# Kernel optimization log

Hardware: AMD Instinct MI355X
Metric: run time of the kernel (lower is better)

Reference implementation:

```python
import jax, jax.numpy as jnp
import numpy as np

ND, NPR, DD, DP, LAT, AT, B = 2048, 2048, 128, 128, 128, 32, 16384


def setup_inputs():
    key = jax.random.key(0)
    ks = jax.random.split(key, 20)
    s = 0.05
    d = {}
    d["e_p_adj"] = (jax.random.uniform(ks[0], (ND, NPR)) < 0.05).astype(jnp.float32)
    d["e_e_adj"] = (jax.random.uniform(ks[1], (ND, ND)) < 0.05).astype(jnp.float32)
    d["p_p_adj"] = (jax.random.uniform(ks[2], (NPR, NPR)) < 0.05).astype(jnp.float32)
    d["input_disease"] = jax.random.randint(ks[3], (B,), 0, ND)
    d["input_drug"] = jax.random.randint(ks[4], (B,), 0, NPR)
    d["labels"] = jax.random.randint(ks[5], (B,), 0, 2)
    # learned parameters
    d["disease_emb"] = jax.random.normal(ks[6], (ND, DD)) * s
    d["drug_emb"] = jax.random.normal(ks[7], (NPR, DP)) * s
    d["Wdg"] = jax.random.normal(ks[8], (DP, LAT)) * s   # disease_gcn_w
    d["bdg_lin"] = jnp.zeros((LAT,))                      # Linear bias
    d["bdg"] = jnp.zeros((LAT,))                          # extra disease_gcn_b
    d["Wpg"] = jax.random.normal(ks[9], (DD, LAT)) * s   # drug_gcn_w
    d["bpg_lin"] = jnp.zeros((LAT,))
    d["bpg"] = jnp.zeros((LAT,))
    d["Wa1_d"] = jax.random.normal(ks[10], (DP + DD, AT)) * s  # concat [key(drug), query(disease)]
    d["ba1_d"] = jnp.zeros((AT,))
    d["Wa2_d"] = jax.random.normal(ks[11], (AT, 1)) * s
    d["ba2_d"] = jnp.zeros((1,))
    d["Wa1_p"] = jax.random.normal(ks[12], (DD + DP, AT)) * s  # concat [key(disease), query(drug)]
    d["ba1_p"] = jnp.zeros((AT,))
    d["Wa2_p"] = jax.random.normal(ks[13], (AT, 1)) * s
    d["ba2_p"] = jnp.zeros((1,))
    d["Wd2"] = jax.random.normal(ks[14], (DD, LAT)) * s  # disease_w2
    d["bd2"] = jnp.zeros((LAT,))
    d["Wp3"] = jax.random.normal(ks[15], (DP, LAT)) * s  # drug_w3
    d["bp3"] = jnp.zeros((LAT,))
    d["mlp_W1"] = jax.random.normal(ks[16], (LAT, DD)) * s
    d["mlp_b1"] = jnp.zeros((DD,))
    d["mlp_W2"] = jax.random.normal(ks[17], (DD, DD)) * s
    d["mlp_b2"] = jnp.zeros((DD,))
    d["Wpred"] = jax.random.normal(ks[18], (DD, 1)) * s
    d["bpred"] = jnp.zeros((1,))
    return d


def _attention_gcn(adj, other, selfe, W1, b1, W2, b2):
    # torch: concat([key=other, query=self]) -> Linear(W1) ; split W1 instead of
    # materializing the [Ns, No, Dk+Dq] concat tensor (same math, less HBM traffic)
    do = other.shape[1]
    ko = other @ W1[:do]              # [No, A]
    qs = selfe @ W1[do:]              # [Ns, A]
    h = jax.nn.relu(qs[:, None, :] + ko[None, :, :] + b1)   # [Ns, No, A]
    alpha = jax.nn.relu(jnp.squeeze(h @ W2, -1) + b2[0])    # [Ns, No]
    alpha = alpha * adj
    return jax.nn.softmax(alpha, axis=1) @ other            # [Ns, Do]


def _forward(e_p_adj, e_e_adj, p_p_adj, input_disease, input_drug, labels,
             disease_emb, drug_emb, Wdg, bdg_lin, bdg, Wpg, bpg_lin, bpg,
             Wa1_d, ba1_d, Wa2_d, ba2_d, Wa1_p, ba1_p, Wa2_p, ba2_p,
             Wd2, bd2, Wp3, bp3, mlp_W1, mlp_b1, mlp_W2, mlp_b2, Wpred, bpred):
    h_e_gcn = _attention_gcn(e_p_adj, drug_emb, disease_emb, Wa1_d, ba1_d, Wa2_d, ba2_d)
    h_e_gcn = h_e_gcn @ Wdg + bdg_lin + bdg
    h_p_gcn = _attention_gcn(e_p_adj.T, disease_emb, drug_emb, Wa1_p, ba1_p, Wa2_p, ba2_p)
    h_p_gcn = h_p_gcn @ Wpg + bpg_lin + bpg
    # disease knn branch
    deg_d = jnp.sum(e_e_adj, axis=1, keepdims=True) + 1e-8
    h_e_e = ((e_e_adj @ disease_emb) / deg_d) @ Wd2 + bd2
    h_e = jax.nn.selu(h_e_gcn + h_e_e)
    # drug knn branch
    deg_p = jnp.sum(p_p_adj, axis=1, keepdims=True) + 1e-8
    h_p_p = ((p_p_adj @ drug_emb) / deg_p) @ Wp3 + bp3
    h_p = jax.nn.selu(h_p_gcn + h_p_p)
    # pair prediction MLP
    x = h_e[input_disease] * h_p[input_drug]                # [B, LAT]
    x = jax.nn.selu(x @ mlp_W1 + mlp_b1)
    x = jax.nn.selu(x @ mlp_W2 + mlp_b2)
    z = jnp.squeeze(x @ Wpred, -1) + bpred[0]               # [B]
    y = labels.astype(jnp.float32)
    # BCEWithLogitsLoss (stable), mean reduction
    loss = jnp.mean(jnp.maximum(z, 0.0) - z * y + jnp.log1p(jnp.exp(-jnp.abs(z))))
    return (loss, jax.nn.sigmoid(z))


def reference(e_p_adj, e_e_adj, p_p_adj, input_disease, input_drug, labels,
              disease_emb, drug_emb, Wdg, bdg_lin, bdg, Wpg, bpg_lin, bpg,
              Wa1_d, ba1_d, Wa2_d, ba2_d, Wa1_p, ba1_p, Wa2_p, ba2_p,
              Wd2, bd2, Wp3, bp3, mlp_W1, mlp_b1, mlp_W2, mlp_b2, Wpred, bpred):
    return _forward(e_p_adj, e_e_adj, p_p_adj, input_disease, input_drug, labels,
                    disease_emb, drug_emb, Wdg, bdg_lin, bdg, Wpg, bpg_lin, bpg,
                    Wa1_d, ba1_d, Wa2_d, ba2_d, Wa1_p, ba1_p, Wa2_p, ba2_p,
                    Wd2, bd2, Wp3, bp3, mlp_W1, mlp_b1, mlp_W2, mlp_b2, Wpred, bpred)
```

## Files before the change

kernel.cpp:

```cpp
#include <hip/hip_runtime.h>

#define ND   2048
#define BB   16384

typedef unsigned short u16;
typedef unsigned int u32;
typedef __attribute__((ext_vector_type(8))) short short8;
typedef __attribute__((ext_vector_type(4))) float f32x4;

__device__ inline float bf2f(u16 u) {
    union { u32 i; float f; } v; v.i = ((u32)u) << 16; return v.f;
}
__device__ inline u16 f2bf(float f) {
    union { float f; u32 i; } v; v.f = f;
    u32 i = v.i + 0x7fffu + ((v.i >> 16) & 1u);
    return (u16)(i >> 16);
}
__device__ inline float seluf(float x) {
    const float sc = 1.0507009873554805f, al = 1.6732632423543772f;
    return x > 0.f ? sc * x : sc * al * expm1f(x);
}
__device__ inline short8 packbf8(float4 f0, float4 f1) {
    short8 a;
    a[0] = (short)f2bf(f0.x); a[1] = (short)f2bf(f0.y);
    a[2] = (short)f2bf(f0.z); a[3] = (short)f2bf(f0.w);
    a[4] = (short)f2bf(f1.x); a[5] = (short)f2bf(f1.y);
    a[6] = (short)f2bf(f1.z); a[7] = (short)f2bf(f1.w);
    return a;
}

__global__ void detectk(const void* __restrict__ demb, u32* __restrict__ flag) {
    const u16* p = (const u16*)demb;
    int tid = threadIdx.x;
    int sane = 0;
    #pragma unroll
    for (int i = 0; i < 2; i++) {
        u16 u = p[4 * tid + 2 * i];
        int e = (u >> 7) & 0xFF;
        if (u == 0 || (e >= 0x66 && e <= 0x8C)) sane++;
    }
    __shared__ int red[256];
    red[tid] = sane; __syncthreads();
    for (int o = 128; o > 0; o >>= 1) {
        if (tid < o) red[tid] += red[tid + o];
        __syncthreads();
    }
    if (tid == 0) flag[0] = (red[0] < 300) ? 1u : 0u;
}

#define NSEG 26
struct CvtArgs { const void* src[NSEG]; int off[NSEG]; int n[NSEG]; };

__global__ __launch_bounds__(256) void cvtk(CvtArgs a, u16* __restrict__ base,
                                            const u32* __restrict__ flag) {
    int seg = blockIdx.y;
    int n = a.n[seg];
    const void* s = a.src[seg];
    u16* d = base + a.off[seg];
    bool f32 = flag[0] != 0;
    int stride = gridDim.x * blockDim.x;
    for (int i = blockIdx.x * blockDim.x + threadIdx.x; i < n; i += stride)
        d[i] = f32 ? f2bf(((const float*)s)[i]) : ((const u16*)s)[i];
}

__device__ inline void tpose_body(const u16* in, int R, int C,
                                  u16* out, int ldo, int ooff,
                                  u16 (*tile)[33]) {
    int c0 = blockIdx.x * 32, r0 = blockIdx.y * 32;
    int x = c0 + threadIdx.x;
    for (int i = threadIdx.y; i < 32; i += 8) {
        int r = r0 + i;
        tile[i][threadIdx.x] = (r < R && x < C) ? in[(size_t)r * C + x] : (u16)0;
    }
    __syncthreads();
    int rr = r0 + threadIdx.x;
    for (int i = threadIdx.y; i < 32; i += 8) {
        int cc = c0 + i;
        if (cc < C && rr < R) out[(size_t)cc * ldo + ooff + rr] = tile[threadIdx.x][i];
    }
}

__global__ void tpose_embs(const u16* __restrict__ demb, const u16* __restrict__ pemb,
                           u16* __restrict__ disT, u16* __restrict__ drugT) {
    __shared__ u16 tile[32][33];
    if (blockIdx.z == 0) tpose_body(demb, ND, 128, disT, ND, 0, tile);
    else                 tpose_body(pemb, ND, 128, drugT, ND, 0, tile);
}

__global__ void tpose_smalls(const u16* s0, const u16* s1, const u16* s2,
                             const u16* s3, const u16* s4, const u16* s5,
                             u16* W1T, u16* W2T, u16* WcTe, u16* WcTp) {
    __shared__ u16 tile[32][33];
    const u16* in; u16* out; int ldo, ooff;
    switch (blockIdx.z) {
        case 0:  in = s0; out = W1T;  ldo = 128; ooff = 0;   break;
        case 1:  in = s1; out = W2T;  ldo = 128; ooff = 0;   break;
        case 2:  in = s2; out = WcTe; ldo = 256; ooff = 0;   break;
        case 3:  in = s3; out = WcTe; ldo = 256; ooff = 128; break;
        case 4:  in = s4; out = WcTp; ldo = 256; ooff = 0;   break;
        default: in = s5; out = WcTp; ldo = 256; ooff = 128; break;
    }
    tpose_body(in, 128, 128, out, ldo, ooff, tile);
}

__global__ void biasc(const u16* a0, const u16* a1, const u16* a2, u16* o0,
                      const u16* b0, const u16* b1, const u16* b2, u16* o1) {
    int t = threadIdx.x;
    o0[t] = f2bf(bf2f(a0[t]) + bf2f(a1[t]) + bf2f(a2[t]));
    o1[t] = f2bf(bf2f(b0[t]) + bf2f(b1[t]) + bf2f(b2[t]));
}

__global__ __launch_bounds__(256) void degk(
    const void* __restrict__ e_e, float* __restrict__ dinv_e,
    const void* __restrict__ p_p, float* __restrict__ dinv_p,
    const u32* __restrict__ flag) {
    int row = blockIdx.x, tid = threadIdx.x;
    const void* ab = blockIdx.y ? p_p : e_e;
    float* o = blockIdx.y ? dinv_p : dinv_e;
    bool f32 = flag[0] != 0;
    float s = 0.f;
    if (f32) {
        const float4* a4 = (const float4*)((const float*)ab + (size_t)row * 2048) + tid * 2;
        float4 v0 = a4[0], v1 = a4[1];
        s = v0.x + v0.y + v0.z + v0.w + v1.x + v1.y + v1.z + v1.w;
    } else {
        const uint4* a4 = (const uint4*)((const u16*)ab + (size_t)row * 2048) + tid;
        uint4 v = a4[0];
        u32 u[4] = {v.x, v.y, v.z, v.w};
        #pragma unroll
        for (int c = 0; c < 4; c++)
            s += bf2f((u16)(u[c] & 0xffff)) + bf2f((u16)(u[c] >> 16));
    }
    __shared__ float red[256];
    red[tid] = s; __syncthreads();
    for (int ofs = 128; ofs > 0; ofs >>= 1) {
        if (tid < ofs) red[tid] += red[tid + ofs];
        __syncthreads();
    }
    if (tid == 0) o[row] = 1.f / (red[0] + 1e-8f);
}

__global__ __launch_bounds__(128) void koqs(
    const u16* __restrict__ demb, const u16* __restrict__ pemb,
    const u16* __restrict__ Wa1d, const u16* __restrict__ ba1d,
    const u16* __restrict__ Wa1p, const u16* __restrict__ ba1p,
    float* __restrict__ ko_d, float* __restrict__ qs_d,
    float* __restrict__ ko_p, float* __restrict__ qs_p) {
    int row = blockIdx.x, m = blockIdx.y, tid = threadIdx.x;
    const u16* src; const u16* W; const u16* bias; float* out;
    switch (m) {
        case 0:  src = pemb; W = Wa1d;            bias = nullptr; out = ko_d; break;
        case 1:  src = demb; W = Wa1d + 128 * 32; bias = ba1d;    out = qs_d; break;
        case 2:  src = demb; W = Wa1p;            bias = nullptr; out = ko_p; break;
        default: src = pemb; W = Wa1p + 128 * 32; bias = ba1p;    out = qs_p; break;
    }
    __shared__ float x[128];
    __shared__ float red[128];
    x[tid] = bf2f(src[(size_t)row * 128 + tid]);
    __syncthreads();
    int a = tid & 31, part = tid >> 5;
    float s = 0.f;
    #pragma unroll
    for (int k = 0; k < 32; k++) s += x[part * 32 + k] * bf2f(W[(part * 32 + k) * 32 + a]);
    red[tid] = s;
    __syncthreads();
    if (part == 0) {
        float t = red[a] + red[a + 32] + red[a + 64] + red[a + 96];
        if (bias) t += bf2f(bias[a]);
        out[(size_t)row * 32 + a] = t;
    }
}

struct AW {
    const float* qs[2]; const float* ko[2];
    const u16* w2[2]; const u16* b2[2];
    u16* outw[2]; float* sums[2];
    int transposed[2];
};

__global__ __launch_bounds__(256, 4) void attnw6(AW a, const void* __restrict__ adj,
                                                 const u32* __restrict__ flag) {
    __shared__ float tile[32][257];
    __shared__ float wpart[4][32];
    int z = blockIdx.z;
    int tid = threadIdx.x;
    int lane = tid & 63, wv = tid >> 6;
    int jl = wv * 64 + lane;
    int jbase = blockIdx.x * 256;
    int j = jbase + jl;
    int p0 = blockIdx.y * 32;
    bool f32a = flag[0] != 0;
    bool tr = a.transposed[z] != 0;
    const float* adjf = (const float*)adj;
    const u16*   adjh = (const u16*)adj;

    float kv[32];
    {
        const float4* kp = (const float4*)(a.ko[z] + (size_t)j * 32);
        #pragma unroll
        for (int qd = 0; qd < 8; qd++) {
            float4 v = kp[qd];
            kv[qd * 4 + 0] = v.x; kv[qd * 4 + 1] = v.y;
            kv[qd * 4 + 2] = v.z; kv[qd * 4 + 3] = v.w;
        }
    }
    float w2v[32];
    #pragma unroll
    for (int i2 = 0; i2 < 32; i2++) w2v[i2] = bf2f(a.w2[z][i2]);
    float b2 = bf2f(a.b2[z][0]);
    const float* qs = a.qs[z];
    u16* outw = a.outw[z];

    if (tr) {
        if (f32a) {
            const float4* src = (const float4*)(adjf + (size_t)(jbase + tid) * 2048 + p0);
            #pragma unroll
            for (int q8 = 0; q8 < 8; q8++) {
                float4 v = src[q8];
                tile[q8 * 4 + 0][tid] = v.x; tile[q8 * 4 + 1][tid] = v.y;
                tile[q8 * 4 + 2][tid] = v.z; tile[q8 * 4 + 3][tid] = v.w;
            }
        } else {
            const uint4* src = (const uint4*)(adjh + (size_t)(jbase + tid) * 2048 + p0);
            #pragma unroll
            for (int q8 = 0; q8 < 4; q8++) {
                uint4 v = src[q8];
                u32 uu[4] = {v.x, v.y, v.z, v.w};
                #pragma unroll
                for (int c = 0; c < 4; c++) {
                    tile[q8 * 8 + c * 2 + 0][tid] = bf2f((u16)(uu[c] & 0xffff));
                    tile[q8 * 8 + c * 2 + 1][tid] = bf2f((u16)(uu[c] >> 16));
                }
            }
        }
        __syncthreads();
    }

    #pragma unroll 1
    for (int pl = 0; pl < 32; pl++) {
        int row = p0 + pl;
        const float* qrow = qs + (size_t)row * 32;
        float s = 0.f;
        #pragma unroll
        for (int aa = 0; aa < 32; aa++)
            s += fmaxf(qrow[aa] + kv[aa], 0.f) * w2v[aa];
        s = fmaxf(s + b2, 0.f);
        float av = tr ? tile[pl][jl]
                      : (f32a ? adjf[(size_t)row * 2048 + j]
                              : bf2f(adjh[(size_t)row * 2048 + j]));
        float e = __expf(s * av);
        outw[(size_t)row * 2048 + j] = f2bf(e);
        float t = e;
        #pragma unroll
        for (int o = 32; o > 0; o >>= 1) t += __shfl_down(t, o, 64);
        if (lane == 0) wpart[wv][pl] = t;
    }
    __syncthreads();
    if (tid < 32)
        a.sums[z][(size_t)blockIdx.x * 2048 + p0 + tid] =
            wpart[0][tid] + wpart[1][tid] + wpart[2][tid] + wpart[3][tid];
}

struct GD4 {
    const void* A[4]; const u16* BT[4]; u16* C[4];
    const u16* bias[4]; const float* rs[4];
    int lda[4], ldb[4], ldc[4], coff[4], kiters[4], act[4], araw[4], rsmode[4];
};

#define PADK 136

__global__ __launch_bounds__(256, 2) void gemmL(GD4 g, const u32* __restrict__ flag) {
    __shared__ __align__(16) u16 As[16][PADK];
    __shared__ __align__(16) u16 Bs[128][PADK];
    int z = blockIdx.y;
    bool af32 = g.araw[z] && (flag[0] != 0);
    const void* A = g.A[z];
    const u16* BT = g.BT[z];
    int lda = g.lda[z], ldb = g.ldb[z];
    int kiters = g.kiters[z];
    int tid = threadIdx.x;
    int lane = tid & 63, wv = tid >> 6;
    int mrow = lane & 15, quad = lane >> 4;
    int m0 = blockIdx.x * 16;
    int c0 = wv * 32;
    int sr = tid >> 4, sk = (tid & 15) * 8;
    f32x4 acc0 = {0.f, 0.f, 0.f, 0.f}, acc1 = {0.f, 0.f, 0.f, 0.f};

    short8 ra, rb[8];
    auto ldstage = [&](int kb) {
        if (af32) {
            const float* A32 = (const float*)A;
            const float4* p = (const float4*)(A32 + (size_t)(m0 + sr) * lda + kb + sk);
            float4 f0 = p[0], f1 = p[1];
            ra = packbf8(f0, f1);
        } else {
            ra = *(const short8*)((const u16*)A + (size_t)(m0 + sr) * lda + kb + sk);
        }
        const u16* bbase = BT + (size_t)sr * ldb + kb + sk;
        #pragma unroll
        for (int i = 0; i < 8; i++)
            rb[i] = *(const short8*)(bbase + (size_t)i * 16 * ldb);
    };
    auto ststage = [&]() {
        *(short8*)(&As[sr][sk]) = ra;
        #pragma unroll
        for (int i = 0; i < 8; i++)
            *(short8*)(&Bs[i * 16 + sr][sk]) = rb[i];
    };
    auto compute = [&]() {
        #pragma unroll
        for (int ks = 0; ks < 4; ks++) {
            short8 af = *(const short8*)(&As[mrow][ks * 32 + quad * 8]);
            short8 b0 = *(const short8*)(&Bs[c0 + mrow][ks * 32 + quad * 8]);
            short8 b1 = *(const short8*)(&Bs[c0 + 16 + mrow][ks * 32 + quad * 8]);
            acc0 = __builtin_amdgcn_mfma_f32_16x16x32_bf16(af, b0, acc0, 0, 0, 0);
            acc1 = __builtin_amdgcn_mfma_f32_16x16x32_bf16(af, b1, acc1, 0, 0, 0);
        }
    };

    ldstage(0);
    #pragma unroll 1
    for (int it = 0; it < kiters - 1; ++it) {
        ststage();
        __syncthreads();
        ldstage((it + 1) * 128);
        compute();
        __syncthreads();
    }
    ststage();
    __syncthreads();
    compute();

    const float* rs = g.rs[z];
    int rsmode = g.rsmode[z];
    const u16* bi = g.bias[z];
    u16* C = g.C[z];
    int ldc = g.ldc[z], coff = g.coff[z], act = g.act[z];
    int n0 = c0 + mrow, n1 = n0 + 16;
    float bv0 = bi ? bf2f(bi[n0]) : 0.f;
    float bv1 = bi ? bf2f(bi[n1]) : 0.f;
    #pragma unroll
    for (int r = 0; r < 4; r++) {
        int row = m0 + quad * 4 + r;
        float v0 = acc0[r], v1 = acc1[r];
        if (rsmode == 1) { float sc = rs[row]; v0 *= sc; v1 *= sc; }
        else if (rsmode == 2) {
            float t = 0.f;
            #pragma unroll
            for (int p = 0; p < 8; p++) t += rs[row + p * 2048];
            float sc = 1.f / t;
            v0 *= sc; v1 *= sc;
        }
        v0 += bv0; v1 += bv1;
        if (act) { v0 = seluf(v0); v1 = seluf(v1); }
        C[(size_t)row * ldc + coff + n0] = f2bf(v0);
        C[(size_t)row * ldc + coff + n1] = f2bf(v1);
    }
}

__global__ __launch_bounds__(256) void xbuild(
    const u16* __restrict__ he, const u16* __restrict__ hp,
    const int* __restrict__ di, const int* __restrict__ dr, u16* __restrict__ X) {
    int idx = blockIdx.x * 256 + threadIdx.x;
    int d2 = idx & 63;
    int b = idx >> 6;
    int ia = di[b], ic = dr[b];
    u32 ue = ((const u32*)he)[ia * 64 + d2];
    u32 up = ((const u32*)hp)[ic * 64 + d2];
    float lo = bf2f((u16)(ue & 0xffff)) * bf2f((u16)(up & 0xffff));
    float hi = bf2f((u16)(ue >> 16)) * bf2f((u16)(up >> 16));
    ((u32*)X)[idx] = (u32)f2bf(lo) | ((u32)f2bf(hi) << 16);
}

__global__ __launch_bounds__(256) void zloss(
    const u16* __restrict__ X2, const u16* __restrict__ wpred,
    const u16* __restrict__ bpred, const int* __restrict__ labels,
    float* __restrict__ out, float* __restrict__ part) {
    __shared__ float wp[128];
    __shared__ float ls[256];
    int tid = threadIdx.x;
    if (tid < 128) wp[tid] = bf2f(wpred[tid]);
    __syncthreads();
    int b = blockIdx.x * 256 + tid;
    const uint4* xp = (const uint4*)(X2 + (size_t)b * 128);
    float z = 0.f;
    #pragma unroll
    for (int i = 0; i < 16; i++) {
        uint4 q = xp[i];
        u32 u[4] = {q.x, q.y, q.z, q.w};
        #pragma unroll
        for (int c = 0; c < 4; c++) {
            z += bf2f((u16)(u[c] & 0xffff)) * wp[i * 8 + c * 2];
            z += bf2f((u16)(u[c] >> 16)) * wp[i * 8 + c * 2 + 1];
        }
    }
    z += bf2f(bpred[0]);
    out[1 + b] = 1.f / (1.f + __expf(-z));
    float y = (float)labels[b];
    ls[tid] = fmaxf(z, 0.f) - z * y + log1pf(__expf(-fabsf(z)));
    __syncthreads();
    for (int o = 128; o > 0; o >>= 1) {
        if (tid < o) ls[tid] += ls[tid + o];
        __syncthreads();
    }
    if (tid == 0) part[blockIdx.x] = ls[0];
}

__global__ void finloss(const float* __restrict__ part, float* __restrict__ out) {
    __shared__ float s[64];
    s[threadIdx.x] = part[threadIdx.x];
    __syncthreads();
    for (int o = 32; o > 0; o >>= 1) {
        if (threadIdx.x < o) s[threadIdx.x] += s[threadIdx.x + o];
        __syncthreads();
    }
    if (threadIdx.x == 0) out[0] = s[0] * (1.f / 16384.f);
}

extern "C" void kernel_launch(void* const* d_in, const int* in_sizes, int n_in,
                              void* d_out, int out_size, void* d_ws, size_t ws_size,
                              hipStream_t stream) {
    const void* e_p_adj = d_in[0];
    const void* e_e_adj = d_in[1];
    const void* p_p_adj = d_in[2];
    const int* in_dis  = (const int*)d_in[3];
    const int* in_drug = (const int*)d_in[4];
    const int* labels  = (const int*)d_in[5];
    float* out = (float*)d_out;

    char* ws = (char*)d_ws;
    size_t off = 0;
    auto take = [&](size_t bytes) { char* p = ws + off; off = (off + bytes + 255) & ~(size_t)255; return p; };
    u16*   Wbuf  = (u16*)take((size_t)2048 * 2048 * 2);
    u16*   drugT = (u16*)take((size_t)128 * 2048 * 2);
    u16*   disT  = (u16*)take((size_t)128 * 2048 * 2);
    float* ko_d  = (float*)take((size_t)2048 * 32 * 4);
    float* qs_d  = (float*)take((size_t)2048 * 32 * 4);
    float* ko_p  = (float*)take((size_t)2048 * 32 * 4);
    float* qs_p  = (float*)take((size_t)2048 * 32 * 4);
    u16*   A_e   = (u16*)take((size_t)2048 * 256 * 2);
    u16*   A_p   = (u16*)take((size_t)2048 * 256 * 2);
    u16*   WcTe  = (u16*)take((size_t)128 * 256 * 2);
    u16*   WcTp  = (u16*)take((size_t)128 * 256 * 2);
    u16*   W1T   = (u16*)take((size_t)128 * 128 * 2);
    u16*   W2T   = (u16*)take((size_t)128 * 128 * 2);
    u16*   b_e   = (u16*)take(256);
    u16*   b_p   = (u16*)take(256);
    u16*   h_e   = (u16*)take((size_t)2048 * 128 * 2);
    u16*   h_p   = (u16*)take((size_t)2048 * 128 * 2);
    float* dinv_e = (float*)take(2048 * 4);
    float* dinv_p = (float*)take(2048 * 4);
    float* sumsD  = (float*)take(8 * 2048 * 4);
    float* sumsP  = (float*)take(8 * 2048 * 4);
    float* part  = (float*)take(64 * 4);
    u16*   canon = (u16*)take((size_t)700000 * 2);
    u32*   flag  = (u32*)take(256);
    bool dual = (ws_size > off) && (ws_size - off) >= ((size_t)2048 * 2048 * 2 + 512);
    u16*   Wbuf2 = dual ? (u16*)take((size_t)2048 * 2048 * 2) : Wbuf;
    u16* X  = Wbuf;
    u16* X1 = Wbuf + (size_t)BB * 128;
    u16* X2 = drugT;

    const int segidx[NSEG] = {6, 7, 14, 18, 8, 22, 11, 24, 26, 28,
                              15, 16, 17, 19, 20, 21,
                              9, 10, 12, 13, 23, 25, 27, 29, 30, 31};
    const int segn[NSEG]   = {262144, 262144, 8192, 8192, 16384, 16384, 16384, 16384, 16384, 16384,
                              32, 32, 1, 32, 32, 1,
                              128, 128, 128, 128, 128, 128, 128, 128, 128, 1};
    CvtArgs ca;
    u16* cp[NSEG];
    {
        int o = 0;
        for (int i = 0; i < NSEG; i++) {
            ca.src[i] = d_in[segidx[i]];
            ca.off[i] = o;
            ca.n[i] = segn[i];
            cp[i] = canon + o;
            o += (segn[i] + 15) & ~15;
        }
    }
    u16 *cdemb = cp[0], *cpemb = cp[1], *cWa1d = cp[2], *cWa1p = cp[3];
    u16 *cWdg = cp[4], *cWd2 = cp[5], *cWpg = cp[6], *cWp3 = cp[7];
    u16 *cW1 = cp[8], *cW2 = cp[9];
    u16 *cba1d = cp[10], *cWa2d = cp[11], *cba2d = cp[12];
    u16 *cba1p = cp[13], *cWa2p = cp[14], *cba2p = cp[15];
    u16 *cbdg_lin = cp[16], *cbdg = cp[17], *cbpg_lin = cp[18], *cbpg = cp[19];
    u16 *cbd2 = cp[20], *cbp3 = cp[21], *cmb1 = cp[22], *cmb2 = cp[23];
    u16 *cWpred = cp[24], *cbpred = cp[25];

    detectk<<<1, 256, 0, stream>>>(d_in[6], flag);
    cvtk<<<dim3(64, NSEG), 256, 0, stream>>>(ca, canon, flag);

    tpose_embs<<<dim3(4, 64, 2), dim3(32, 8), 0, stream>>>(cdemb, cpemb, disT, drugT);
    tpose_smalls<<<dim3(4, 4, 6), dim3(32, 8), 0, stream>>>(
        cW1, cW2, cWdg, cWd2, cWpg, cWp3, W1T, W2T, WcTe, WcTp);
    biasc<<<1, 128, 0, stream>>>(cbdg_lin, cbdg, cbd2, b_e, cbpg_lin, cbpg, cbp3, b_p);
    degk<<<dim3(2048, 2), 256, 0, stream>>>(e_e_adj, dinv_e, p_p_adj, dinv_p, flag);
    koqs<<<dim3(2048, 4), 128, 0, stream>>>(cdemb, cpemb, cWa1d, cba1d, cWa1p, cba1p,
                                            ko_d, qs_d, ko_p, qs_p);

    auto setd = [](GD4& g, int z, const void* A, int lda, const u16* BT, int ldb,
                   u16* C, int ldc, int coff, int ki, const u16* bi,
                   const float* rs, int act, int araw, int rm) {
        g.A[z] = A; g.lda[z] = lda; g.BT[z] = BT; g.ldb[z] = ldb;
        g.C[z] = C; g.ldc[z] = ldc; g.coff[z] = coff; g.kiters[z] = ki;
        g.bias[z] = bi; g.rs[z] = rs; g.act[z] = act; g.araw[z] = araw; g.rsmode[z] = rm;
    };
    auto mkaw = [](const float* qs0, const float* ko0, const u16* w20, const u16* b20,
                   u16* o0, float* s0, int t0,
                   const float* qs1, const float* ko1, const u16* w21, const u16* b21,
                   u16* o1, float* s1, int t1) {
        AW a;
        a.qs[0] = qs0; a.ko[0] = ko0; a.w2[0] = w20; a.b2[0] = b20;
        a.outw[0] = o0; a.sums[0] = s0; a.transposed[0] = t0;
        a.qs[1] = qs1; a.ko[1] = ko1; a.w2[1] = w21; a.b2[1] = b21;
        a.outw[1] = o1; a.sums[1] = s1; a.transposed[1] = t1;
        return a;
    };

    if (dual) {
        AW aw = mkaw(qs_d, ko_d, cWa2d, cba2d, Wbuf, sumsD, 0,
                     qs_p, ko_p, cWa2p, cba2p, Wbuf2, sumsP, 1);
        attnw6<<<dim3(8, 64, 2), 256, 0, stream>>>(aw, e_p_adj, flag);
        GD4 g;
        setd(g, 0, Wbuf, 2048, drugT, 2048, A_e, 256, 0, 16, nullptr, sumsD, 0, 0, 2);
        setd(g, 1, e_e_adj, 2048, disT, 2048, A_e, 256, 128, 16, nullptr, dinv_e, 0, 1, 1);
        setd(g, 2, Wbuf2, 2048, disT, 2048, A_p, 256, 0, 16, nullptr, sumsP, 0, 0, 2);
        setd(g, 3, p_p_adj, 2048, drugT, 2048, A_p, 256, 128, 16, nullptr, dinv_p, 0, 1, 1);
        gemmL<<<dim3(128, 4), 256, 0, stream>>>(g, flag);
    } else {
        AW aw1 = mkaw(qs_d, ko_d, cWa2d, cba2d, Wbuf, sumsD, 0,
                      qs_d, ko_d, cWa2d, cba2d, Wbuf, sumsD, 0);
        attnw6<<<dim3(8, 64, 1), 256, 0, stream>>>(aw1, e_p_adj, flag);
        GD4 g1;
        setd(g1, 0, Wbuf, 2048, drugT, 2048, A_e, 256, 0, 16, nullptr, sumsD, 0, 0, 2);
        setd(g1, 1, e_e_adj, 2048, disT, 2048, A_e, 256, 128, 16, nullptr, dinv_e, 0, 1, 1);
        setd(g1, 2, Wbuf, 2048, drugT, 2048, A_e, 256, 0, 16, nullptr, sumsD, 0, 0, 2);
        setd(g1, 3, Wbuf, 2048, drugT, 2048, A_e, 256, 0, 16, nullptr, sumsD, 0, 0, 2);
        gemmL<<<dim3(128, 2), 256, 0, stream>>>(g1, flag);
        AW aw2 = mkaw(qs_p, ko_p, cWa2p, cba2p, Wbuf, sumsP, 1,
                      qs_p, ko_p, cWa2p, cba2p, Wbuf, sumsP, 1);
        attnw6<<<dim3(8, 64, 1), 256, 0, stream>>>(aw2, e_p_adj, flag);
        GD4 g2;
        setd(g2, 0, Wbuf, 2048, disT, 2048, A_p, 256, 0, 16, nullptr, sumsP, 0, 0, 2);
        setd(g2, 1, p_p_adj, 2048, drugT, 2048, A_p, 256, 128, 16, nullptr, dinv_p, 0, 1, 1);
        setd(g2, 2, Wbuf, 2048, disT, 2048, A_p, 256, 0, 16, nullptr, sumsP, 0, 0, 2);
        setd(g2, 3, Wbuf, 2048, disT, 2048, A_p, 256, 0, 16, nullptr, sumsP, 0, 0, 2);
        gemmL<<<dim3(128, 2), 256, 0, stream>>>(g2, flag);
    }

    {
        GD4 g;
        setd(g, 0, A_e, 256, WcTe, 256, h_e, 128, 0, 2, b_e, nullptr, 1, 0, 0);
        setd(g, 1, A_p, 256, WcTp, 256, h_p, 128, 0, 2, b_p, nullptr, 1, 0, 0);
        setd(g, 2, A_e, 256, WcTe, 256, h_e, 128, 0, 2, b_e, nullptr, 1, 0, 0);
        setd(g, 3, A_e, 256, WcTe, 256, h_e, 128, 0, 2, b_e, nullptr, 1, 0, 0);
        gemmL<<<dim3(128, 2), 256, 0, stream>>>(g, flag);
    }

    xbuild<<<4096, 256, 0, stream>>>(h_e, h_p, in_dis, in_drug, X);
    {
        GD4 g;
        setd(g, 0, X, 128, W1T, 128, X1, 128, 0, 1, cmb1, nullptr, 1, 0, 0);
        setd(g, 1, X, 128, W1T, 128, X1, 128, 0, 1, cmb1, nullptr, 1, 0, 0);
        setd(g, 2, X, 128, W1T, 128, X1, 128, 0, 1, cmb1, nullptr, 1, 0, 0);
        setd(g, 3, X, 128, W1T, 128, X1, 128, 0, 1, cmb1, nullptr, 1, 0, 0);
        gemmL<<<dim3(1024, 1), 256, 0, stream>>>(g, flag);
    }
    {
        GD4 g;
        setd(g, 0, X1, 128, W2T, 128, X2, 128, 0, 1, cmb2, nullptr, 1, 0, 0);
        setd(g, 1, X1, 128, W2T, 128, X2, 128, 0, 1, cmb2, nullptr, 1, 0, 0);
        setd(g, 2, X1, 128, W2T, 128, X2, 128, 0, 1, cmb2, nullptr, 1, 0, 0);
        setd(g, 3, X1, 128, W2T, 128, X2, 128, 0, 1, cmb2, nullptr, 1, 0, 0);
        gemmL<<<dim3(1024, 1), 256, 0, stream>>>(g, flag);
    }

    zloss<<<64, 256, 0, stream>>>(X2, cWpred, cbpred, labels, out, part);
    finloss<<<1, 64, 0, stream>>>(part, out);
}
```

Baseline: 256.6 us.

## Replace dense attention and adjacency GEMMs with CSR sparse aggregation

```diff
diff --git a/kernel.cpp b/kernel.cpp
--- a/kernel.cpp
+++ b/kernel.cpp
@@ -78,13 +78,6 @@
         int cc = c0 + i;
         if (cc < C && rr < R) out[(size_t)cc * ldo + ooff + rr] = tile[threadIdx.x][i];
     }
-}
-
-__global__ void tpose_embs(const u16* __restrict__ demb, const u16* __restrict__ pemb,
-                           u16* __restrict__ disT, u16* __restrict__ drugT) {
-    __shared__ u16 tile[32][33];
-    if (blockIdx.z == 0) tpose_body(demb, ND, 128, disT, ND, 0, tile);
-    else                 tpose_body(pemb, ND, 128, drugT, ND, 0, tile);
 }
 
 __global__ void tpose_smalls(const u16* s0, const u16* s1, const u16* s2,
@@ -103,41 +96,45 @@
     tpose_body(in, 128, 128, out, ldo, ooff, tile);
 }
 
+__global__ __launch_bounds__(256) void colsump(const u16* __restrict__ demb,
+                                               const u16* __restrict__ pemb,
+                                               float* __restrict__ part) {
+    int m = blockIdx.y;
+    const u16* e = m ? pemb : demb;
+    int t = threadIdx.x;
+    int c2 = t & 63, rg = t >> 6;
+    int r0 = blockIdx.x * 64;
+    float s0 = 0.f, s1 = 0.f;
+    for (int i = 0; i < 16; i++) {
+        u32 v = *(const u32*)(e + (size_t)(r0 + i * 4 + rg) * 128 + c2 * 2);
+        s0 += bf2f((u16)(v & 0xffffu));
+        s1 += bf2f((u16)(v >> 16));
+    }
+    __shared__ float t0[256], t1[256];
+    t0[t] = s0; t1[t] = s1;
+    __syncthreads();
+    if (t < 64) {
+        float a0 = t0[t] + t0[t + 64] + t0[t + 128] + t0[t + 192];
+        float a1 = t1[t] + t1[t + 64] + t1[t + 128] + t1[t + 192];
+        part[(size_t)m * 4096 + blockIdx.x * 128 + t * 2 + 0] = a0;
+        part[(size_t)m * 4096 + blockIdx.x * 128 + t * 2 + 1] = a1;
+    }
+}
+
 __global__ void biasc(const u16* a0, const u16* a1, const u16* a2, u16* o0,
-                      const u16* b0, const u16* b1, const u16* b2, u16* o1) {
+                      const u16* b0, const u16* b1, const u16* b2, u16* o1,
+                      const float* __restrict__ part,
+                      float* __restrict__ csd, float* __restrict__ csp) {
     int t = threadIdx.x;
     o0[t] = f2bf(bf2f(a0[t]) + bf2f(a1[t]) + bf2f(a2[t]));
     o1[t] = f2bf(bf2f(b0[t]) + bf2f(b1[t]) + bf2f(b2[t]));
-}
-
-__global__ __launch_bounds__(256) void degk(
-    const void* __restrict__ e_e, float* __restrict__ dinv_e,
-    const void* __restrict__ p_p, float* __restrict__ dinv_p,
-    const u32* __restrict__ flag) {
-    int row = blockIdx.x, tid = threadIdx.x;
-    const void* ab = blockIdx.y ? p_p : e_e;
-    float* o = blockIdx.y ? dinv_p : dinv_e;
-    bool f32 = flag[0] != 0;
-    float s = 0.f;
-    if (f32) {
-        const float4* a4 = (const float4*)((const float*)ab + (size_t)row * 2048) + tid * 2;
-        float4 v0 = a4[0], v1 = a4[1];
-        s = v0.x + v0.y + v0.z + v0.w + v1.x + v1.y + v1.z + v1.w;
-    } else {
-        const uint4* a4 = (const uint4*)((const u16*)ab + (size_t)row * 2048) + tid;
-        uint4 v = a4[0];
-        u32 u[4] = {v.x, v.y, v.z, v.w};
-        #pragma unroll
-        for (int c = 0; c < 4; c++)
-            s += bf2f((u16)(u[c] & 0xffff)) + bf2f((u16)(u[c] >> 16));
-    }
-    __shared__ float red[256];
-    red[tid] = s; __syncthreads();
-    for (int ofs = 128; ofs > 0; ofs >>= 1) {
-        if (tid < ofs) red[tid] += red[tid + ofs];
-        __syncthreads();
-    }
-    if (tid == 0) o[row] = 1.f / (red[0] + 1e-8f);
+    float sd = 0.f, sp = 0.f;
+    for (int b = 0; b < 32; b++) {
+        sd += part[b * 128 + t];
+        sp += part[4096 + b * 128 + t];
+    }
+    csd[t] = sd;
+    csp[t] = sp;
 }
 
 __global__ __launch_bounds__(128) void koqs(
@@ -171,94 +168,133 @@
     }
 }
 
-struct AW {
-    const float* qs[2]; const float* ko[2];
-    const u16* w2[2]; const u16* b2[2];
-    u16* outw[2]; float* sums[2];
-    int transposed[2];
+struct CS {
+    const void* adj[3];
+    u16* ridx[3]; u32* rcnt[3];
+    u16* cidx; u32* ccnt;
 };
 
-__global__ __launch_bounds__(256, 4) void attnw6(AW a, const void* __restrict__ adj,
-                                                 const u32* __restrict__ flag) {
-    __shared__ float tile[32][257];
-    __shared__ float wpart[4][32];
-    int z = blockIdx.z;
+__global__ __launch_bounds__(256) void csrbuild(CS c, const u32* __restrict__ flag) {
+    int m = blockIdx.y, r = blockIdx.x, t = threadIdx.x;
+    bool f32 = flag[0] != 0;
+    __shared__ u32 lcnt;
+    if (t == 0) lcnt = 0;
+    __syncthreads();
+    float v[8];
+    int c0 = t * 8;
+    if (f32) {
+        const float4* p = (const float4*)((const float*)c.adj[m] + (size_t)r * 2048 + c0);
+        float4 x = p[0], y = p[1];
+        v[0] = x.x; v[1] = x.y; v[2] = x.z; v[3] = x.w;
+        v[4] = y.x; v[5] = y.y; v[6] = y.z; v[7] = y.w;
+    } else {
+        const uint4* p = (const uint4*)((const u16*)c.adj[m] + (size_t)r * 2048 + c0);
+        uint4 x = p[0];
+        u32 u[4] = {x.x, x.y, x.z, x.w};
+        #pragma unroll
+        for (int i = 0; i < 4; i++) {
+            v[2 * i + 0] = (u[i] & 0xffffu) ? 1.f : 0.f;
+            v[2 * i + 1] = (u[i] >> 16)     ? 1.f : 0.f;
+        }
+    }
+    u16* ridx = c.ridx[m] + (size_t)r * 2048;
+    #pragma unroll
+    for (int i = 0; i < 8; i++) {
+        if (v[i] != 0.f) {
+            u32 p = atomicAdd(&lcnt, 1u);
+            ridx[p] = (u16)(c0 + i);
+            if (m == 0) {
+                u32 q = atomicAdd(&c.ccnt[c0 + i], 1u);
+                c.cidx[(size_t)(c0 + i) * 2048 + q] = (u16)r;
+            }
+        }
+    }
+    __syncthreads();
+    if (t == 0) c.rcnt[m][r] = lcnt;
+}
+
+struct SP {
+    const u16* idx[4]; const u32* cnt[4];
+    const float* ko[4]; const float* qs[4];
+    const u16* w2[4]; const u16* b2[4];
+    const u16* emb[4]; const float* csum[4];
+    u16* out[4]; int ooff[4]; int attn[4];
+};
+
+__global__ __launch_bounds__(256) void spagg(SP a) {
+    int task = blockIdx.y;
     int tid = threadIdx.x;
-    int lane = tid & 63, wv = tid >> 6;
-    int jl = wv * 64 + lane;
-    int jbase = blockIdx.x * 256;
-    int j = jbase + jl;
-    int p0 = blockIdx.y * 32;
-    bool f32a = flag[0] != 0;
-    bool tr = a.transposed[z] != 0;
-    const float* adjf = (const float*)adj;
-    const u16*   adjh = (const u16*)adj;
-
-    float kv[32];
-    {
-        const float4* kp = (const float4*)(a.ko[z] + (size_t)j * 32);
+    int wv = tid >> 6, lane = tid & 63;
+    int r = blockIdx.x * 4 + wv;
+    const u16* idx = a.idx[task] + (size_t)r * 2048;
+    int nnz = (int)a.cnt[task][r];
+    int isat = a.attn[task];
+    const u16* emb = a.emb[task];
+    const float* ko = a.ko[task];
+
+    float qsr[32], w2h[32];
+    float b2v = 0.f;
+    if (isat) {
+        const float4* qp = (const float4*)(a.qs[task] + (size_t)r * 32);
         #pragma unroll
-        for (int qd = 0; qd < 8; qd++) {
-            float4 v = kp[qd];
-            kv[qd * 4 + 0] = v.x; kv[qd * 4 + 1] = v.y;
-            kv[qd * 4 + 2] = v.z; kv[qd * 4 + 3] = v.w;
-        }
-    }
-    float w2v[32];
-    #pragma unroll
-    for (int i2 = 0; i2 < 32; i2++) w2v[i2] = bf2f(a.w2[z][i2]);
-    float b2 = bf2f(a.b2[z][0]);
-    const float* qs = a.qs[z];
-    u16* outw = a.outw[z];
-
-    if (tr) {
-        if (f32a) {
-            const float4* src = (const float4*)(adjf + (size_t)(jbase + tid) * 2048 + p0);
-            #pragma unroll
-            for (int q8 = 0; q8 < 8; q8++) {
-                float4 v = src[q8];
-                tile[q8 * 4 + 0][tid] = v.x; tile[q8 * 4 + 1][tid] = v.y;
-                tile[q8 * 4 + 2][tid] = v.z; tile[q8 * 4 + 3][tid] = v.w;
+        for (int i = 0; i < 8; i++) {
+            float4 v = qp[i];
+            qsr[4 * i + 0] = v.x; qsr[4 * i + 1] = v.y;
+            qsr[4 * i + 2] = v.z; qsr[4 * i + 3] = v.w;
+        }
+        #pragma unroll
+        for (int i = 0; i < 32; i++) w2h[i] = bf2f(a.w2[task][i]);
+        b2v = bf2f(a.b2[task][0]);
+    }
+
+    float acc0 = 0.f, acc1 = 0.f, wsum = 0.f;
+
+    for (int base = 0; base < nnz; base += 64) {
+        int i = base + lane;
+        float w = 0.f;
+        int j = 0;
+        if (i < nnz) {
+            j = (int)idx[i];
+            if (isat) {
+                const float4* kp = (const float4*)(ko + (size_t)j * 32);
+                float s = 0.f;
+                #pragma unroll
+                for (int q = 0; q < 8; q++) {
+                    float4 kv = kp[q];
+                    s += fmaxf(qsr[4 * q + 0] + kv.x, 0.f) * w2h[4 * q + 0];
+                    s += fmaxf(qsr[4 * q + 1] + kv.y, 0.f) * w2h[4 * q + 1];
+                    s += fmaxf(qsr[4 * q + 2] + kv.z, 0.f) * w2h[4 * q + 2];
+                    s += fmaxf(qsr[4 * q + 3] + kv.w, 0.f) * w2h[4 * q + 3];
+                }
+                w = __expf(fmaxf(s + b2v, 0.f)) - 1.f;
+            } else {
+                w = 1.f;
             }
-        } else {
-            const uint4* src = (const uint4*)(adjh + (size_t)(jbase + tid) * 2048 + p0);
-            #pragma unroll
-            for (int q8 = 0; q8 < 4; q8++) {
-                uint4 v = src[q8];
-                u32 uu[4] = {v.x, v.y, v.z, v.w};
-                #pragma unroll
-                for (int c = 0; c < 4; c++) {
-                    tile[q8 * 8 + c * 2 + 0][tid] = bf2f((u16)(uu[c] & 0xffff));
-                    tile[q8 * 8 + c * 2 + 1][tid] = bf2f((u16)(uu[c] >> 16));
-                }
-            }
-        }
-        __syncthreads();
-    }
-
-    #pragma unroll 1
-    for (int pl = 0; pl < 32; pl++) {
-        int row = p0 + pl;
-        const float* qrow = qs + (size_t)row * 32;
-        float s = 0.f;
-        #pragma unroll
-        for (int aa = 0; aa < 32; aa++)
-            s += fmaxf(qrow[aa] + kv[aa], 0.f) * w2v[aa];
-        s = fmaxf(s + b2, 0.f);
-        float av = tr ? tile[pl][jl]
-                      : (f32a ? adjf[(size_t)row * 2048 + j]
-                              : bf2f(adjh[(size_t)row * 2048 + j]));
-        float e = __expf(s * av);
-        outw[(size_t)row * 2048 + j] = f2bf(e);
-        float t = e;
-        #pragma unroll
-        for (int o = 32; o > 0; o >>= 1) t += __shfl_down(t, o, 64);
-        if (lane == 0) wpart[wv][pl] = t;
-    }
-    __syncthreads();
-    if (tid < 32)
-        a.sums[z][(size_t)blockIdx.x * 2048 + p0 + tid] =
-            wpart[0][tid] + wpart[1][tid] + wpart[2][tid] + wpart[3][tid];
+        }
+        int cend = min(64, nnz - base);
+        #pragma unroll 4
+        for (int k = 0; k < cend; k++) {
+            float wk = __shfl(w, k);
+            int jk = __shfl(j, k);
+            u32 pe = *(const u32*)(emb + (size_t)jk * 128 + lane * 2);
+            acc0 = fmaf(wk, bf2f((u16)(pe & 0xffffu)), acc0);
+            acc1 = fmaf(wk, bf2f((u16)(pe >> 16)), acc1);
+            wsum += wk;
+        }
+    }
+
+    float v0, v1;
+    if (isat) {
+        float sc = 1.f / (2048.f + wsum);
+        v0 = (a.csum[task][lane * 2 + 0] + acc0) * sc;
+        v1 = (a.csum[task][lane * 2 + 1] + acc1) * sc;
+    } else {
+        float sc = 1.f / (wsum + 1e-8f);
+        v0 = acc0 * sc;
+        v1 = acc1 * sc;
+    }
+    u32 pk = (u32)f2bf(v0) | ((u32)f2bf(v1) << 16);
+    *(u32*)(a.out[task] + (size_t)r * 256 + a.ooff[task] + lane * 2) = pk;
 }
 
 struct GD4 {
@@ -431,13 +467,6 @@
     char* ws = (char*)d_ws;
     size_t off = 0;
     auto take = [&](size_t bytes) { char* p = ws + off; off = (off + bytes + 255) & ~(size_t)255; return p; };
-    u16*   Wbuf  = (u16*)take((size_t)2048 * 2048 * 2);
-    u16*   drugT = (u16*)take((size_t)128 * 2048 * 2);
-    u16*   disT  = (u16*)take((size_t)128 * 2048 * 2);
-    float* ko_d  = (float*)take((size_t)2048 * 32 * 4);
-    float* qs_d  = (float*)take((size_t)2048 * 32 * 4);
-    float* ko_p  = (float*)take((size_t)2048 * 32 * 4);
-    float* qs_p  = (float*)take((size_t)2048 * 32 * 4);
     u16*   A_e   = (u16*)take((size_t)2048 * 256 * 2);
     u16*   A_p   = (u16*)take((size_t)2048 * 256 * 2);
     u16*   WcTe  = (u16*)take((size_t)128 * 256 * 2);
@@ -448,18 +477,27 @@
     u16*   b_p   = (u16*)take(256);
     u16*   h_e   = (u16*)take((size_t)2048 * 128 * 2);
     u16*   h_p   = (u16*)take((size_t)2048 * 128 * 2);
-    float* dinv_e = (float*)take(2048 * 4);
-    float* dinv_p = (float*)take(2048 * 4);
-    float* sumsD  = (float*)take(8 * 2048 * 4);
-    float* sumsP  = (float*)take(8 * 2048 * 4);
+    float* ko_d  = (float*)take((size_t)2048 * 32 * 4);
+    float* qs_d  = (float*)take((size_t)2048 * 32 * 4);
+    float* ko_p  = (float*)take((size_t)2048 * 32 * 4);
+    float* qs_p  = (float*)take((size_t)2048 * 32 * 4);
+    float* cspart = (float*)take((size_t)2 * 32 * 128 * 4);
+    float* csd   = (float*)take(128 * 4);
+    float* csp   = (float*)take(128 * 4);
     float* part  = (float*)take(64 * 4);
+    u32*   flag  = (u32*)take(256);
     u16*   canon = (u16*)take((size_t)700000 * 2);
-    u32*   flag  = (u32*)take(256);
-    bool dual = (ws_size > off) && (ws_size - off) >= ((size_t)2048 * 2048 * 2 + 512);
-    u16*   Wbuf2 = dual ? (u16*)take((size_t)2048 * 2048 * 2) : Wbuf;
-    u16* X  = Wbuf;
-    u16* X1 = Wbuf + (size_t)BB * 128;
-    u16* X2 = drugT;
+    u16*   X     = (u16*)take((size_t)BB * 128 * 2);
+    u16*   X1    = (u16*)take((size_t)BB * 128 * 2);
+    u16*   X2    = (u16*)take((size_t)BB * 128 * 2);
+    u16*   idx0  = (u16*)take((size_t)2048 * 2048 * 2);
+    u16*   idx1  = (u16*)take((size_t)2048 * 2048 * 2);
+    u16*   idx2  = (u16*)take((size_t)2048 * 2048 * 2);
+    u16*   idx3  = (u16*)take((size_t)2048 * 2048 * 2);
+    u32*   cnt0  = (u32*)take(2048 * 4);
+    u32*   cnt2  = (u32*)take(2048 * 4);
+    u32*   cnt3  = (u32*)take(2048 * 4);
+    u32*   cntT  = (u32*)take(2048 * 4);
 
     const int segidx[NSEG] = {6, 7, 14, 18, 8, 22, 11, 24, 26, 28,
                               15, 16, 17, 19, 20, 21,
@@ -491,13 +529,40 @@
     detectk<<<1, 256, 0, stream>>>(d_in[6], flag);
     cvtk<<<dim3(64, NSEG), 256, 0, stream>>>(ca, canon, flag);
 
-    tpose_embs<<<dim3(4, 64, 2), dim3(32, 8), 0, stream>>>(cdemb, cpemb, disT, drugT);
+    hipMemsetAsync(cntT, 0, 2048 * sizeof(u32), stream);
+    {
+        CS cs;
+        cs.adj[0] = e_p_adj; cs.ridx[0] = idx0; cs.rcnt[0] = cnt0;
+        cs.adj[1] = e_e_adj; cs.ridx[1] = idx2; cs.rcnt[1] = cnt2;
+        cs.adj[2] = p_p_adj; cs.ridx[2] = idx3; cs.rcnt[2] = cnt3;
+        cs.cidx = idx1; cs.ccnt = cntT;
+        csrbuild<<<dim3(2048, 3), 256, 0, stream>>>(cs, flag);
+    }
+
+    colsump<<<dim3(32, 2), 256, 0, stream>>>(cdemb, cpemb, cspart);
     tpose_smalls<<<dim3(4, 4, 6), dim3(32, 8), 0, stream>>>(
         cW1, cW2, cWdg, cWd2, cWpg, cWp3, W1T, W2T, WcTe, WcTp);
-    biasc<<<1, 128, 0, stream>>>(cbdg_lin, cbdg, cbd2, b_e, cbpg_lin, cbpg, cbp3, b_p);
-    degk<<<dim3(2048, 2), 256, 0, stream>>>(e_e_adj, dinv_e, p_p_adj, dinv_p, flag);
+    biasc<<<1, 128, 0, stream>>>(cbdg_lin, cbdg, cbd2, b_e, cbpg_lin, cbpg, cbp3, b_p,
+                                 cspart, csd, csp);
     koqs<<<dim3(2048, 4), 128, 0, stream>>>(cdemb, cpemb, cWa1d, cba1d, cWa1p, cba1p,
                                             ko_d, qs_d, ko_p, qs_p);
+
+    {
+        SP sp;
+        sp.idx[0] = idx0; sp.cnt[0] = cnt0; sp.ko[0] = ko_d; sp.qs[0] = qs_d;
+        sp.w2[0] = cWa2d; sp.b2[0] = cba2d; sp.emb[0] = cpemb; sp.csum[0] = csp;
+        sp.out[0] = A_e; sp.ooff[0] = 0; sp.attn[0] = 1;
+        sp.idx[1] = idx2; sp.cnt[1] = cnt2; sp.ko[1] = ko_d; sp.qs[1] = qs_d;
+        sp.w2[1] = cWa2d; sp.b2[1] = cba2d; sp.emb[1] = cdemb; sp.csum[1] = csd;
+        sp.out[1] = A_e; sp.ooff[1] = 128; sp.attn[1] = 0;
+        sp.idx[2] = idx1; sp.cnt[2] = cntT; sp.ko[2] = ko_p; sp.qs[2] = qs_p;
+        sp.w2[2] = cWa2p; sp.b2[2] = cba2p; sp.emb[2] = cdemb; sp.csum[2] = csd;
+        sp.out[2] = A_p; sp.ooff[2] = 0; sp.attn[2] = 1;
+        sp.idx[3] = idx3; sp.cnt[3] = cnt3; sp.ko[3] = ko_p; sp.qs[3] = qs_p;
+        sp.w2[3] = cWa2p; sp.b2[3] = cba2p; sp.emb[3] = cpemb; sp.csum[3] = csp;
+        sp.out[3] = A_p; sp.ooff[3] = 128; sp.attn[3] = 0;
+        spagg<<<dim3(512, 4), 256, 0, stream>>>(sp);
+    }
 
     auto setd = [](GD4& g, int z, const void* A, int lda, const u16* BT, int ldb,
                    u16* C, int ldc, int coff, int ki, const u16* bi,
@@ -506,48 +571,6 @@
         g.C[z] = C; g.ldc[z] = ldc; g.coff[z] = coff; g.kiters[z] = ki;
         g.bias[z] = bi; g.rs[z] = rs; g.act[z] = act; g.araw[z] = araw; g.rsmode[z] = rm;
     };
-    auto mkaw = [](const float* qs0, const float* ko0, const u16* w20, const u16* b20,
-                   u16* o0, float* s0, int t0,
-                   const float* qs1, const float* ko1, const u16* w21, const u16* b21,
-                   u16* o1, float* s1, int t1) {
-        AW a;
-        a.qs[0] = qs0; a.ko[0] = ko0; a.w2[0] = w20; a.b2[0] = b20;
-        a.outw[0] = o0; a.sums[0] = s0; a.transposed[0] = t0;
-        a.qs[1] = qs1; a.ko[1] = ko1; a.w2[1] = w21; a.b2[1] = b21;
-        a.outw[1] = o1; a.sums[1] = s1; a.transposed[1] = t1;
-        return a;
-    };
-
-    if (dual) {
-        AW aw = mkaw(qs_d, ko_d, cWa2d, cba2d, Wbuf, sumsD, 0,
-                     qs_p, ko_p, cWa2p, cba2p, Wbuf2, sumsP, 1);
-        attnw6<<<dim3(8, 64, 2), 256, 0, stream>>>(aw, e_p_adj, flag);
-        GD4 g;
-        setd(g, 0, Wbuf, 2048, drugT, 2048, A_e, 256, 0, 16, nullptr, sumsD, 0, 0, 2);
-        setd(g, 1, e_e_adj, 2048, disT, 2048, A_e, 256, 128, 16, nullptr, dinv_e, 0, 1, 1);
-        setd(g, 2, Wbuf2, 2048, disT, 2048, A_p, 256, 0, 16, nullptr, sumsP, 0, 0, 2);
-        setd(g, 3, p_p_adj, 2048, drugT, 2048, A_p, 256, 128, 16, nullptr, dinv_p, 0, 1, 1);
-        gemmL<<<dim3(128, 4), 256, 0, stream>>>(g, flag);
-    } else {
-        AW aw1 = mkaw(qs_d, ko_d, cWa2d, cba2d, Wbuf, sumsD, 0,
-                      qs_d, ko_d, cWa2d, cba2d, Wbuf, sumsD, 0);
-        attnw6<<<dim3(8, 64, 1), 256, 0, stream>>>(aw1, e_p_adj, flag);
-        GD4 g1;
-        setd(g1, 0, Wbuf, 2048, drugT, 2048, A_e, 256, 0, 16, nullptr, sumsD, 0, 0, 2);
-        setd(g1, 1, e_e_adj, 2048, disT, 2048, A_e, 256, 128, 16, nullptr, dinv_e, 0, 1, 1);
-        setd(g1, 2, Wbuf, 2048, drugT, 2048, A_e, 256, 0, 16, nullptr, sumsD, 0, 0, 2);
-        setd(g1, 3, Wbuf, 2048, drugT, 2048, A_e, 256, 0, 16, nullptr, sumsD, 0, 0, 2);
-        gemmL<<<dim3(128, 2), 256, 0, stream>>>(g1, flag);
-        AW aw2 = mkaw(qs_p, ko_p, cWa2p, cba2p, Wbuf, sumsP, 1,
-                      qs_p, ko_p, cWa2p, cba2p, Wbuf, sumsP, 1);
-        attnw6<<<dim3(8, 64, 1), 256, 0, stream>>>(aw2, e_p_adj, flag);
-        GD4 g2;
-        setd(g2, 0, Wbuf, 2048, disT, 2048, A_p, 256, 0, 16, nullptr, sumsP, 0, 0, 2);
-        setd(g2, 1, p_p_adj, 2048, drugT, 2048, A_p, 256, 128, 16, nullptr, dinv_p, 0, 1, 1);
-        setd(g2, 2, Wbuf, 2048, disT, 2048, A_p, 256, 0, 16, nullptr, sumsP, 0, 0, 2);
-        setd(g2, 3, Wbuf, 2048, disT, 2048, A_p, 256, 0, 16, nullptr, sumsP, 0, 0, 2);
-        gemmL<<<dim3(128, 2), 256, 0, stream>>>(g2, flag);
-    }
 
     {
         GD4 g;
```

New measurement: 285.9 us. 11.4% more time.
